# Performance work log

Measured on AMD Instinct MI355X. Metric: run time of the kernel, lower is better.

The kernel has to match this reference:

```python
import jax, jax.numpy as jnp
import numpy as np

B, T, D, H = 8, 4096, 1024, 16
DK = D // H
CHUNK = 64
E, TOPK, MULT, CAPF = 8, 2, 4, 1.25
HID = D * MULT
N = B * T
CAPACITY = int(CAPF * (N / E))  # 5120


def setup_inputs() -> dict:
    key = jax.random.key(0)
    ks = jax.random.split(key, 16)
    s = 0.02
    r = lambda k, shape: jax.random.normal(k, shape, jnp.float32) * s
    return {
        "x": jax.random.normal(ks[0], (B, T, D), jnp.float32),
        "norm1_scale": jnp.ones((D,), jnp.float32),
        "norm2_scale": jnp.ones((D,), jnp.float32),
        "Wq": r(ks[1], (D, D)), "bq": jnp.zeros((D,), jnp.float32),
        "Wk": r(ks[2], (D, D)), "bk": jnp.zeros((D,), jnp.float32),
        "Wv": r(ks[3], (D, D)), "bv": jnp.zeros((D,), jnp.float32),
        "Wg": r(ks[4], (D, D)), "bg": jnp.zeros((D,), jnp.float32),
        "Wo": r(ks[5], (D, D)), "bo": jnp.zeros((D,), jnp.float32),
        "router_W": r(ks[6], (D, E)), "router_b": jnp.zeros((E,), jnp.float32),
        "W1": r(ks[7], (E, D, HID)), "b1": jnp.zeros((E, HID), jnp.float32),
        "W2": r(ks[8], (E, HID, D)), "b2": jnp.zeros((E, D), jnp.float32),
    }


def rmsnorm(x, scale):
    # torch: x / (||x|| / sqrt(d)) * scale == x * rsqrt(mean(x^2)) * scale (no eps)
    return x / jnp.sqrt(jnp.mean(x * x, axis=-1, keepdims=True)) * scale


def apply_rope(x):
    # x: (B, H, T, DK); non-interleaved half-rotation as in source
    half = x.shape[-1] // 2
    t = x.shape[2]
    inv = 1.0 / (10000.0 ** (jnp.arange(half, dtype=jnp.float32) / half))
    ang = jnp.arange(t, dtype=jnp.float32)[:, None] * inv[None, :]  # (T, half)
    sin, cos = jnp.sin(ang)[None, None], jnp.cos(ang)[None, None]
    x1, x2 = x[..., :half], x[..., half:]
    return jnp.concatenate([x1 * cos - x2 * sin, x1 * sin + x2 * cos], axis=-1)


def phi(x):
    return jax.nn.elu(x) + 1.0


def attention(x, Wq, bq, Wk, bk, Wv, bv, Wg, bg, Wo, bo):
    b, t, c = x.shape
    heads = lambda y: y.reshape(b, t, H, DK).transpose(0, 2, 1, 3)  # (B,H,T,DK)
    q = phi(apply_rope(heads(x @ Wq + bq)))
    k = phi(apply_rope(heads(x @ Wk + bk)))
    v = heads(x @ Wv + bv)
    g = heads(jax.nn.sigmoid(x @ Wg + bg))
    nc = t // CHUNK
    to_chunks = lambda y: y.reshape(b, H, nc, CHUNK, DK).transpose(2, 0, 1, 3, 4)
    qs, ks_, vs, gs = map(to_chunks, (q, k, v, g))  # (nc,B,H,chunk,DK)
    S0 = jnp.zeros((b, H, DK, DK), x.dtype)
    Z0 = jnp.zeros((b, H, DK), x.dtype)

    def step(carry, inp):
        S, Z = carry
        qc, kc, vc, gc = inp
        S = S + jnp.einsum('bhtd,bhte->bhde', kc, vc)
        Z = Z + kc.sum(axis=2)
        num = jnp.einsum('bhtd,bhde->bhte', qc, S)
        den = jnp.einsum('bhtd,bhd->bht', qc, Z)[..., None] + 1e-6
        return (S, Z), gc * (num / den)

    _, outs = jax.lax.scan(step, (S0, Z0), (qs, ks_, vs, gs))  # (nc,B,H,chunk,DK)
    out = outs.transpose(1, 2, 0, 3, 4).reshape(b, H, t, DK)
    out = out.transpose(0, 2, 1, 3).reshape(b, t, c)
    return out @ Wo + bo


def moe(x, router_W, router_b, W1, b1, W2, b2):
    b, t, c = x.shape
    n = b * t
    xf = x.reshape(n, c)
    probs = jax.nn.softmax(xf @ router_W + router_b, axis=-1)
    topk_probs, topk_idx = jax.lax.top_k(probs, TOPK)
    topk_probs = topk_probs / topk_probs.sum(axis=-1, keepdims=True)
    out = jnp.zeros_like(xf)
    load = []
    for eid in range(E):  # fixed small expert loop (matches source structure)
        mask = (topk_idx == eid).reshape(-1)  # row-major == torch.where order
        idx = jnp.nonzero(mask, size=CAPACITY, fill_value=n * TOPK)[0]
        valid = idx < n * TOPK
        idxc = jnp.minimum(idx, n * TOPK - 1)
        tok, choice = idxc // TOPK, idxc % TOPK
        h = jax.nn.gelu(xf[tok] @ W1[eid] + b1[eid], approximate=False) @ W2[eid] + b2[eid]
        gate = jnp.where(valid, topk_probs[tok, choice], 0.0)
        out = out.at[tok].add(gate[:, None] * h)  # invalid slots have gate==0
        load.append(jnp.minimum(mask.sum(), CAPACITY).astype(xf.dtype))
    load = jnp.stack(load)
    importance = probs.sum(axis=0)
    importance = importance / importance.sum()
    load = load / load.sum()
    aux = (importance * load).sum() * (E ** 2)
    return out.reshape(b, t, c), aux


def reference(x, norm1_scale, norm2_scale, Wq, bq, Wk, bk, Wv, bv, Wg, bg, Wo, bo,
              router_W, router_b, W1, b1, W2, b2):
    x = x + attention(rmsnorm(x, norm1_scale), Wq, bq, Wk, bk, Wv, bv, Wg, bg, Wo, bo)
    moe_out, aux = moe(rmsnorm(x, norm2_scale), router_W, router_b, W1, b1, W2, b2)
    return (x + moe_out, aux)
```

## Files before the change

kernel.cpp:

```cpp
#include <hip/hip_runtime.h>
#include <hip/hip_bf16.h>

#define NTOK 32768
#define TSEQ 4096
#define DM   1024
#define NHEAD 16
#define NEXP 8
#define CAPE 5120
#define HIDN 4096
#define GTOK 8192
#define KSPL 5120

#ifndef __has_builtin
#define __has_builtin(x) 0
#endif
#if __has_builtin(__builtin_amdgcn_global_load_lds)
#define HAVE_GLOAD 1
#else
#define HAVE_GLOAD 0
#endif

typedef __attribute__((ext_vector_type(8))) short bf16x8;
typedef __attribute__((ext_vector_type(4))) float f32x4;

__device__ __forceinline__ float phi_f(float v) { return v > 0.f ? v + 1.f : expf(v); }

__device__ __forceinline__ unsigned short f2bf_bits(float f) {
    __hip_bfloat16 h = __float2bfloat16(f);
    union { __hip_bfloat16 h; unsigned short s; } u;
    u.h = h;
    return u.s;
}
__device__ __forceinline__ float bf_to_f(unsigned short s) {
    unsigned int u = ((unsigned int)s) << 16;
    union { unsigned int u; float f; } w; w.u = u;
    return w.f;
}

__global__ void k_ws_flag(float* out, float v) { if (threadIdx.x == 0) out[0] = v; }

__global__ void k_zero(int* p, int n) {
    int i = blockIdx.x * 256 + threadIdx.x;
    if (i < n) p[i] = 0;
}

__global__ __launch_bounds__(256) void k_rope_table(float* __restrict__ ct, float* __restrict__ st)
{
    const int idx = blockIdx.x * 256 + threadIdx.x;
    const int t = idx >> 5, j = idx & 31;
    const float inv = (float)(1.0 / pow(10000.0, (double)j / 32.0));
    float sn, cn;
    sincosf((float)t * inv, &sn, &cn);
    ct[idx] = cn; st[idx] = sn;
}

struct WPack { const float* W[5]; };
__global__ __launch_bounds__(256) void k_build_wstack(WPack P, __hip_bfloat16* __restrict__ BTbase)
{
    __shared__ float t_[32][33];
    const int z = blockIdx.z;
    const float* Wm = P.W[z];
    __hip_bfloat16* BT = BTbase + (size_t)z * DM * KSPL;
    const int n0 = blockIdx.x * 32, k0 = blockIdx.y * 32;
    const int c = threadIdx.x & 31, r0 = (threadIdx.x >> 5);
#pragma unroll
    for (int i = 0; i < 4; ++i) { int r = r0 + i * 8; t_[r][c] = Wm[(size_t)(k0 + r) * DM + n0 + c]; }
    __syncthreads();
#pragma unroll
    for (int i = 0; i < 4; ++i) {
        int r = r0 + i * 8;
        float val = t_[c][r];
        unsigned short b0 = f2bf_bits(val);
        float res = val - bf_to_f(b0);
        unsigned short b1 = f2bf_bits(res);
        __hip_bfloat16 h0, h1;
        union { __hip_bfloat16 h; unsigned short s; } u0, u1;
        u0.s = b0; u1.s = b1; h0 = u0.h; h1 = u1.h;
        const size_t nrow = (size_t)(n0 + r) * KSPL + (k0 + c);
        BT[nrow]            = h0;
        BT[nrow + 1024]     = h0;
        BT[nrow + 2048]     = h0;
        BT[nrow + 3072]     = h1;
        BT[nrow + 4096]     = h1;
    }
}

template<bool NORM>
__global__ __launch_bounds__(256) void k_rms_split(const float* __restrict__ X,
                                                   const float* __restrict__ nscale,
                                                   __hip_bfloat16* __restrict__ Xs)
{
    const int row = blockIdx.x;
    const int tid = threadIdx.x;
    const float* xr = X + (size_t)row * DM;
    float4 v = ((const float4*)xr)[tid];
    float r = 1.f;
    if (NORM) {
        float s = v.x * v.x + v.y * v.y + v.z * v.z + v.w * v.w;
        for (int off = 32; off; off >>= 1) s += __shfl_xor(s, off);
        __shared__ float redw[4];
        __shared__ float rbc;
        if ((tid & 63) == 0) redw[tid >> 6] = s;
        __syncthreads();
        if (tid == 0) {
            float tot = redw[0] + redw[1] + redw[2] + redw[3];
            rbc = (float)(1.0 / sqrt((double)tot * (1.0 / 1024.0)));
        }
        __syncthreads();
        r = rbc;
    }
    float c[4] = {v.x, v.y, v.z, v.w};
    if (NORM) {
        float4 ns = ((const float4*)nscale)[tid];
        c[0] *= r * ns.x; c[1] *= r * ns.y; c[2] *= r * ns.z; c[3] *= r * ns.w;
    }
    ushort4 p0, p1, p2;
    unsigned short* q0 = (unsigned short*)&p0;
    unsigned short* q1 = (unsigned short*)&p1;
    unsigned short* q2 = (unsigned short*)&p2;
#pragma unroll
    for (int i = 0; i < 4; ++i) {
        float x = c[i];
        unsigned short b0 = f2bf_bits(x);
        float r1 = x - bf_to_f(b0);
        unsigned short b1 = f2bf_bits(r1);
        float r2 = r1 - bf_to_f(b1);
        unsigned short b2 = f2bf_bits(r2);
        q0[i] = b0; q1[i] = b1; q2[i] = b2;
    }
    __hip_bfloat16* base = Xs + (size_t)row * 3072;
    ((ushort4*)(base))[tid] = p0;
    ((ushort4*)(base + 1024))[tid] = p1;
    ((ushort4*)(base + 2048))[tid] = p2;
}

__global__ __launch_bounds__(256) void k_rmsnorm_stats(const float* __restrict__ X,
                                                       float* __restrict__ rn,
                                                       const float* __restrict__ nscale,
                                                       __hip_bfloat16* __restrict__ xbf)
{
    const int row = blockIdx.x;
    const int tid = threadIdx.x;
    const float* xr = X + (size_t)row * DM;
    float4 v = ((const float4*)xr)[tid];
    float s = v.x * v.x + v.y * v.y + v.z * v.z + v.w * v.w;
    for (int off = 32; off; off >>= 1) s += __shfl_xor(s, off);
    __shared__ float redw[4];
    __shared__ float rbc;
    if ((tid & 63) == 0) redw[tid >> 6] = s;
    __syncthreads();
    if (tid == 0) {
        float tot = redw[0] + redw[1] + redw[2] + redw[3];
        float r = (float)(1.0 / sqrt((double)tot * (1.0 / 1024.0)));
        rn[row] = r; rbc = r;
    }
    __syncthreads();
    float r = rbc;
    float4 ns = ((const float4*)nscale)[tid];
    ushort4 o;
    o.x = f2bf_bits(v.x * r * ns.x);
    o.y = f2bf_bits(v.y * r * ns.y);
    o.z = f2bf_bits(v.z * r * ns.z);
    o.w = f2bf_bits(v.w * r * ns.w);
    ((ushort4*)(xbf + (size_t)row * DM))[tid] = o;
}

#if HAVE_GLOAD
__device__ __forceinline__ void gload16(const __hip_bfloat16* g, __hip_bfloat16* l)
{
    __builtin_amdgcn_global_load_lds((const __attribute__((address_space(1))) unsigned int*)g,
                                     (__attribute__((address_space(3))) unsigned int*)l, 16, 0, 0);
}
#endif

struct ProjPack {
    const __hip_bfloat16* BT[4];
    const float* bias[4];
    float* C[4];
};

template<int NMAT, bool RESID>
__global__ __launch_bounds__(256) void k_gemm_proj(const __hip_bfloat16* __restrict__ A,
                                                   ProjPack P,
                                                   const float* __restrict__ resid)
{
    const int z = (NMAT == 4) ? blockIdx.z : 0;
    const __hip_bfloat16* BT = P.BT[z];
    const float* bias = P.bias[z];
    float* C = P.C[z];
    const int m0 = blockIdx.y * 128;
    const int n0 = blockIdx.x * 128;
    const int tid = threadIdx.x;
    __shared__ alignas(16) __hip_bfloat16 As[128 * 32];
    __shared__ alignas(16) __hip_bfloat16 Bs[128 * 32];

    const int lane = tid & 63, wv = tid >> 6;
    const int lr = lane & 15, lgp = lane >> 4;
    const int wm = (wv >> 1) * 64, wn = (wv & 1) * 64;

#if HAVE_GLOAD
    const int rA0 = wv * 32 + (lane >> 2), rA1 = rA0 + 16;
    const int ch = lane & 3;
    const __hip_bfloat16* srcA0 = A + (size_t)(m0 + rA0) * 3072 + ((ch ^ (rA0 & 3)) * 8);
    const __hip_bfloat16* srcA1 = A + (size_t)(m0 + rA1) * 3072 + ((ch ^ (rA1 & 3)) * 8);
    const __hip_bfloat16* srcB0 = BT + (size_t)(n0 + rA0) * KSPL + ((ch ^ (rA0 & 3)) * 8);
    const __hip_bfloat16* srcB1 = BT + (size_t)(n0 + rA1) * KSPL + ((ch ^ (rA1 & 3)) * 8);
    __hip_bfloat16* ldsA0 = As + (size_t)(wv * 32) * 32;
    __hip_bfloat16* ldsA1 = As + (size_t)(wv * 32 + 16) * 32;
    __hip_bfloat16* ldsB0 = Bs + (size_t)(wv * 32) * 32;
    __hip_bfloat16* ldsB1 = Bs + (size_t)(wv * 32 + 16) * 32;
#else
    const int ar = tid >> 1, ac0 = (tid & 1) * 2;
    const __hip_bfloat16* Arow = A + (size_t)(m0 + ar) * 3072;
    const __hip_bfloat16* Brow = BT + (size_t)(n0 + ar) * KSPL;
#endif

    f32x4 acc[4][4];
#pragma unroll
    for (int i = 0; i < 4; ++i)
#pragma unroll
        for (int j = 0; j < 4; ++j) acc[i][j] = (f32x4){0.f, 0.f, 0.f, 0.f};

    int a_off[4], b_off[4];
#pragma unroll
    for (int i = 0; i < 4; ++i) {
        int mrow = wm + i * 16 + lr;
        a_off[i] = mrow * 32 + ((lgp ^ (mrow & 3)) * 8);
        int nrow = wn + i * 16 + lr;
        b_off[i] = nrow * 32 + ((lgp ^ (nrow & 3)) * 8);
    }

    for (int k0 = 0; k0 < KSPL; k0 += 32) {
        const int acol = (k0 < 3072) ? k0 : (k0 - 3072);
        __syncthreads();
#if HAVE_GLOAD
        gload16(srcA0 + acol, ldsA0);
        gload16(srcA1 + acol, ldsA1);
        gload16(srcB0 + k0, ldsB0);
        gload16(srcB1 + k0, ldsB1);
#else
        {
            uint4 av0 = *(const uint4*)(Arow + acol + ac0 * 8);
            uint4 av1 = *(const uint4*)(Arow + acol + ac0 * 8 + 8);
            uint4 bv0 = *(const uint4*)(Brow + k0 + ac0 * 8);
            uint4 bv1 = *(const uint4*)(Brow + k0 + ac0 * 8 + 8);
            *(uint4*)(As + ar * 32 + ((ac0    ) ^ (ar & 3)) * 8) = av0;
            *(uint4*)(As + ar * 32 + ((ac0 + 1) ^ (ar & 3)) * 8) = av1;
            *(uint4*)(Bs + ar * 32 + ((ac0    ) ^ (ar & 3)) * 8) = bv0;
            *(uint4*)(Bs + ar * 32 + ((ac0 + 1) ^ (ar & 3)) * 8) = bv1;
        }
#endif
        __syncthreads();
        bf16x8 af[4], bfr[4];
#pragma unroll
        for (int i = 0; i < 4; ++i) af[i] = *(const bf16x8*)(As + a_off[i]);
#pragma unroll
        for (int j = 0; j < 4; ++j) bfr[j] = *(const bf16x8*)(Bs + b_off[j]);
#pragma unroll
        for (int i = 0; i < 4; ++i)
#pragma unroll
            for (int j = 0; j < 4; ++j)
                acc[i][j] = __builtin_amdgcn_mfma_f32_16x16x32_bf16(af[i], bfr[j], acc[i][j], 0, 0, 0);
    }

#pragma unroll
    for (int i = 0; i < 4; ++i)
#pragma unroll
        for (int j = 0; j < 4; ++j) {
            const int col = n0 + wn + j * 16 + lr;
            const float bval = bias[col];
#pragma unroll
            for (int r = 0; r < 4; ++r) {
                const int rloc = wm + i * 16 + lgp * 4 + r;
                float v = acc[i][j][r] + bval;
                if (RESID) v += resid[(size_t)(m0 + rloc) * DM + col];
                C[(size_t)(m0 + rloc) * DM + col] = v;
            }
        }
}

__global__ __launch_bounds__(256) void k_scan_kv(float* KS, float* Vz,
                                                 const float* __restrict__ ct,
                                                 const float* __restrict__ st)
{
    const int c = blockIdx.x, bh = blockIdx.y;
    const int h = bh & 15, b = bh >> 4;
    const int tid = threadIdx.x;
    __shared__ float ks[64][68];
    __shared__ float vs[64][68];
    const size_t rowbase = ((size_t)b * TSEQ + c * 64) * DM + h * 64;
#pragma unroll
    for (int p = 0; p < 8; ++p) {
        int idx = p * 256 + tid;
        int t = idx >> 5, j = idx & 31;
        const size_t base = rowbase + (size_t)t * DM + j;
        float cn = ct[(c * 64 + t) * 32 + j];
        float sn = st[(c * 64 + t) * 32 + j];
        float k1 = KS[base], k2 = KS[base + 32];
        ks[t][j]      = phi_f(k1 * cn - k2 * sn);
        ks[t][j + 32] = phi_f(k1 * sn + k2 * cn);
    }
#pragma unroll
    for (int p = 0; p < 4; ++p) {
        int idx = p * 256 + tid;
        int t = idx >> 4, e4 = (idx & 15) * 4;
        *(float4*)&vs[t][e4] = *(const float4*)&Vz[rowbase + (size_t)t * DM + e4];
    }
    __syncthreads();
    const int e = tid & 63, dg = tid >> 6;
    float acc[16] = {};
    for (int t = 0; t < 64; ++t) {
        float vv = vs[t][e];
#pragma unroll
        for (int q = 0; q < 4; ++q) {
            float4 kq = *(const float4*)&ks[t][dg * 16 + q * 4];
            acc[q * 4 + 0] = fmaf(kq.x, vv, acc[q * 4 + 0]);
            acc[q * 4 + 1] = fmaf(kq.y, vv, acc[q * 4 + 1]);
            acc[q * 4 + 2] = fmaf(kq.z, vv, acc[q * 4 + 2]);
            acc[q * 4 + 3] = fmaf(kq.w, vv, acc[q * 4 + 3]);
        }
    }
#pragma unroll
    for (int i = 0; i < 16; ++i) {
        int d = dg * 16 + i;
        KS[rowbase + (size_t)d * DM + e] = acc[i];
    }
    if (tid < 64) {
        float z = 0.f;
        for (int t = 0; t < 64; ++t) z += ks[t][tid];
        Vz[rowbase + tid] = z;
    }
}

__global__ __launch_bounds__(256) void k_scan_prefix(float* S)
{
    const int sg = blockIdx.x, bh = blockIdx.y;
    const int h = bh & 15, b = bh >> 4;
    const int idx = sg * 256 + threadIdx.x;
    const int d = idx >> 6, e = idx & 63;
    const size_t base = (size_t)b * TSEQ * DM + h * 64 + (size_t)d * DM + e;
    float acc = 0.f;
    for (int c = 0; c < 64; ++c) {
        size_t p = base + (size_t)c * 64 * DM;
        acc += S[p];
        S[p] = acc;
    }
}

__global__ void k_zprefix(float* Vz)
{
    const int bh = blockIdx.x;
    const int h = bh & 15, b = bh >> 4;
    const int d = threadIdx.x;
    const size_t base = (size_t)b * TSEQ * DM + h * 64 + d;
    float acc = 0.f;
    for (int c = 0; c < 64; ++c) {
        size_t p = base + (size_t)c * 64 * DM;
        acc += Vz[p];
        Vz[p] = acc;
    }
}

__global__ __launch_bounds__(256) void k_scan_out(const float* __restrict__ Q,
                                                  const float* __restrict__ S,
                                                  const float* __restrict__ Zv,
                                                  float* GO,
                                                  const float* __restrict__ ct,
                                                  const float* __restrict__ st)
{
    const int c = blockIdx.x, bh = blockIdx.y;
    const int h = bh & 15, b = bh >> 4;
    const int tid = threadIdx.x;
    __shared__ float qs[64][69];
    __shared__ float Ss[64][68];
    __shared__ float den[64], Zl[64];
    const size_t rowbase = ((size_t)b * TSEQ + c * 64) * DM + h * 64;
#pragma unroll
    for (int p = 0; p < 8; ++p) {
        int idx = p * 256 + tid;
        int t = idx >> 5, j = idx & 31;
        const size_t base = rowbase + (size_t)t * DM + j;
        float cn = ct[(c * 64 + t) * 32 + j];
        float sn = st[(c * 64 + t) * 32 + j];
        float q1 = Q[base], q2 = Q[base + 32];
        qs[t][j]      = phi_f(q1 * cn - q2 * sn);
        qs[t][j + 32] = phi_f(q1 * sn + q2 * cn);
    }
#pragma unroll
    for (int p = 0; p < 4; ++p) {
        int idx = p * 256 + tid;
        int d = idx >> 4, e4 = (idx & 15) * 4;
        *(float4*)&Ss[d][e4] = *(const float4*)&S[rowbase + (size_t)d * DM + e4];
    }
    const int e = tid & 63, tg = tid >> 6;
    float greg[16];
#pragma unroll
    for (int i = 0; i < 16; ++i)
        greg[i] = GO[rowbase + (size_t)(tg * 16 + i) * DM + e];
    if (tid < 64) Zl[tid] = Zv[rowbase + tid];
    __syncthreads();
    if (tid < 64) {
        float dd = 0.f;
        for (int d = 0; d < 64; ++d) dd += qs[tid][d] * Zl[d];
        den[tid] = dd + 1e-6f;
    }
    __syncthreads();
    float acc[16] = {};
    for (int d = 0; d < 64; ++d) {
        float sv = Ss[d][e];
#pragma unroll
        for (int i = 0; i < 16; ++i)
            acc[i] = fmaf(qs[tg * 16 + i][d], sv, acc[i]);
    }
#pragma unroll
    for (int i = 0; i < 16; ++i) {
        int t = tg * 16 + i;
        float g = 1.f / (1.f + expf(-greg[i]));
        GO[rowbase + (size_t)t * DM + e] = g * acc[i] / den[t];
    }
}

__global__ __launch_bounds__(256) void k_router(const float* __restrict__ X2,
                                                const float* __restrict__ rn2,
                                                const float* __restrict__ ns2,
                                                const float* __restrict__ rW,
                                                const float* __restrict__ rb,
                                                int* __restrict__ route_e,
                                                float* __restrict__ route_g,
                                                float* __restrict__ probs)
{
    const int tok = blockIdx.x * 4 + (threadIdx.x >> 6);
    const int lane = threadIdx.x & 63;
    const float* xr = X2 + (size_t)tok * DM;
    const float rn = rn2[tok];
    float lg[8] = {};
    for (int d = lane; d < DM; d += 64) {
        float xv = xr[d] * rn * ns2[d];
        const float4* w4 = (const float4*)(rW + (size_t)d * 8);
        float4 w0 = w4[0], w1 = w4[1];
        lg[0] += xv * w0.x; lg[1] += xv * w0.y; lg[2] += xv * w0.z; lg[3] += xv * w0.w;
        lg[4] += xv * w1.x; lg[5] += xv * w1.y; lg[6] += xv * w1.z; lg[7] += xv * w1.w;
    }
#pragma unroll
    for (int e = 0; e < 8; ++e)
        for (int off = 32; off; off >>= 1) lg[e] += __shfl_xor(lg[e], off);
    if (lane == 0) {
        float pe[8]; float mx = -1e30f, s = 0.f;
#pragma unroll
        for (int e = 0; e < 8; ++e) { lg[e] += rb[e]; mx = fmaxf(mx, lg[e]); }
#pragma unroll
        for (int e = 0; e < 8; ++e) { pe[e] = expf(lg[e] - mx); s += pe[e]; }
#pragma unroll
        for (int e = 0; e < 8; ++e) { pe[e] /= s; probs[(size_t)tok * 8 + e] = pe[e]; }
        int i1 = 0; float p1 = pe[0];
#pragma unroll
        for (int e = 1; e < 8; ++e) if (pe[e] > p1) { p1 = pe[e]; i1 = e; }
        int i2 = -1; float p2 = -1.f;
#pragma unroll
        for (int e = 0; e < 8; ++e) if (e != i1 && pe[e] > p2) { p2 = pe[e]; i2 = e; }
        const float gsum = p1 + p2;
        route_e[tok * 2] = i1; route_e[tok * 2 + 1] = i2;
        route_g[tok * 2] = p1 / gsum; route_g[tok * 2 + 1] = p2 / gsum;
    }
}

__global__ __launch_bounds__(256) void k_count(const int* __restrict__ route_e, int* __restrict__ bcnt)
{
    __shared__ int c[8];
    const int tid = threadIdx.x;
    if (tid < 8) c[tid] = 0;
    __syncthreads();
    atomicAdd(&c[route_e[blockIdx.x * 256 + tid]], 1);
    __syncthreads();
    if (tid < 8) bcnt[blockIdx.x * 8 + tid] = c[tid];
}

__global__ void k_scan_blocks(const int* __restrict__ bcnt, int* __restrict__ bbase, int* __restrict__ ctot)
{
    const int e = threadIdx.x;
    if (e < 8) {
        int run = 0;
        for (int b = 0; b < 256; ++b) { bbase[b * 8 + e] = run; run += bcnt[b * 8 + e]; }
        ctot[e] = run;
    }
}

__global__ __launch_bounds__(256) void k_place(const int* __restrict__ route_e,
                                               const float* __restrict__ route_g,
                                               const int* __restrict__ bbase,
                                               int* __restrict__ tokslot,
                                               float* __restrict__ gateslot)
{
    const int tid = threadIdx.x;
    const int a = blockIdx.x * 256 + tid;
    const int e = route_e[a];
    __shared__ int se[256];
    se[tid] = e;
    __syncthreads();
    int rank = 0;
    for (int j = 0; j < tid; ++j) rank += (se[j] == e) ? 1 : 0;
    const int slot = bbase[blockIdx.x * 8 + e] + rank;
    if (slot < CAPE) {
        tokslot[e * CAPE + slot] = a >> 1;
        gateslot[e * CAPE + slot] = route_g[a];
    }
}

__global__ __launch_bounds__(256) void k_aux(const float* __restrict__ probs,
                                             const int* __restrict__ ctot,
                                             float* __restrict__ out_aux)
{
    const int tid = threadIdx.x;
    float part[8] = {};
    for (int i = tid; i < NTOK; i += 256) {
        const float* p = probs + (size_t)i * 8;
#pragma unroll
        for (int e = 0; e < 8; ++e) part[e] += p[e];
    }
    __shared__ float red[256];
    __shared__ float accs[8];
    for (int e = 0; e < 8; ++e) {
        red[tid] = part[e];
        __syncthreads();
        for (int s = 128; s; s >>= 1) { if (tid < s) red[tid] += red[tid + s]; __syncthreads(); }
        if (tid == 0) accs[e] = red[0];
        __syncthreads();
    }
    if (tid == 0) {
        float isum = 0.f, lsum = 0.f, l[8];
        for (int e = 0; e < 8; ++e) isum += accs[e];
        for (int e = 0; e < 8; ++e) { l[e] = fminf((float)ctot[e], (float)CAPE); lsum += l[e]; }
        float aux = 0.f;
        for (int e = 0; e < 8; ++e) aux += (accs[e] / isum) * (l[e] / lsum);
        out_aux[0] = aux * 64.f;
    }
}

__global__ void k_transpose_bf16(const float* __restrict__ src, __hip_bfloat16* __restrict__ dst,
                                 int K_, int N_)
{
    __shared__ float t_[32][33];
    const int z = blockIdx.z;
    const float* s = src + (size_t)z * K_ * N_;
    __hip_bfloat16* d = dst + (size_t)z * K_ * N_;
    const int n0 = blockIdx.x * 32, k0 = blockIdx.y * 32;
    const int c = threadIdx.x, r0 = threadIdx.y;
#pragma unroll
    for (int i = 0; i < 4; ++i) { int r = r0 + i * 8; t_[r][c] = s[(size_t)(k0 + r) * N_ + n0 + c]; }
    __syncthreads();
#pragma unroll
    for (int i = 0; i < 4; ++i) { int r = r0 + i * 8; d[(size_t)(n0 + r) * K_ + k0 + c] = __float2bfloat16(t_[c][r]); }
}

template<int MODE>
__global__ __launch_bounds__(256) void k_gemm_bf16(const __hip_bfloat16* __restrict__ A,
                                                   const __hip_bfloat16* __restrict__ BT,
                                                   const float* __restrict__ bias,
                                                   __hip_bfloat16* __restrict__ Hout,
                                                   float* __restrict__ Fout,
                                                   const int* __restrict__ tokslot,
                                                   const float* __restrict__ gateslot,
                                                   int K, int Nout, int e0)
{
    const int le = blockIdx.z;
    const int e = e0 + le;
    const int m0 = blockIdx.y * 128;
    const int n0 = blockIdx.x * 128;
    const int tid = threadIdx.x;
    __shared__ alignas(16) __hip_bfloat16 As[128 * 32];
    __shared__ alignas(16) __hip_bfloat16 Bs[128 * 32];
    __shared__ int s_tok[128];
    __shared__ float s_gate[128];
    if (tid < 128) {
        s_tok[tid] = tokslot[e * CAPE + m0 + tid];
        s_gate[tid] = gateslot[e * CAPE + m0 + tid];
    }
    __syncthreads();

    const int lane = tid & 63, wv = tid >> 6;
    const int lr = lane & 15, lgp = lane >> 4;
    const int wm = (wv >> 1) * 64, wn = (wv & 1) * 64;

#if HAVE_GLOAD
    const int rA0 = wv * 32 + (lane >> 2), rA1 = rA0 + 16;
    const int ch = lane & 3;
    const __hip_bfloat16 *srcA0, *srcA1;
    if (MODE == 0) {
        srcA0 = A + (size_t)s_tok[rA0] * K + ((ch ^ (rA0 & 3)) * 8);
        srcA1 = A + (size_t)s_tok[rA1] * K + ((ch ^ (rA1 & 3)) * 8);
    } else {
        srcA0 = A + ((size_t)le * CAPE + m0 + rA0) * K + ((ch ^ (rA0 & 3)) * 8);
        srcA1 = A + ((size_t)le * CAPE + m0 + rA1) * K + ((ch ^ (rA1 & 3)) * 8);
    }
    const __hip_bfloat16* srcB0 = BT + ((size_t)e * Nout + n0 + rA0) * K + ((ch ^ (rA0 & 3)) * 8);
    const __hip_bfloat16* srcB1 = BT + ((size_t)e * Nout + n0 + rA1) * K + ((ch ^ (rA1 & 3)) * 8);
    __hip_bfloat16* ldsA0 = As + (size_t)(wv * 32) * 32;
    __hip_bfloat16* ldsA1 = As + (size_t)(wv * 32 + 16) * 32;
    __hip_bfloat16* ldsB0 = Bs + (size_t)(wv * 32) * 32;
    __hip_bfloat16* ldsB1 = Bs + (size_t)(wv * 32 + 16) * 32;
#else
    const int ar = tid >> 1, ac0 = (tid & 1) * 2;
    const __hip_bfloat16* Arow;
    if (MODE == 0) Arow = A + (size_t)s_tok[ar] * K;
    else           Arow = A + ((size_t)le * CAPE + m0 + ar) * K;
    const __hip_bfloat16* Brow = BT + ((size_t)e * Nout + n0 + ar) * K;
#endif

    f32x4 acc[4][4];
#pragma unroll
    for (int i = 0; i < 4; ++i)
#pragma unroll
        for (int j = 0; j < 4; ++j) acc[i][j] = (f32x4){0.f, 0.f, 0.f, 0.f};

    int a_off[4], b_off[4];
#pragma unroll
    for (int i = 0; i < 4; ++i) {
        int mrow = wm + i * 16 + lr;
        a_off[i] = mrow * 32 + ((lgp ^ (mrow & 3)) * 8);
        int nrow = wn + i * 16 + lr;
        b_off[i] = nrow * 32 + ((lgp ^ (nrow & 3)) * 8);
    }

    for (int k0 = 0; k0 < K; k0 += 32) {
        __syncthreads();
#if HAVE_GLOAD
        gload16(srcA0 + k0, ldsA0);
        gload16(srcA1 + k0, ldsA1);
        gload16(srcB0 + k0, ldsB0);
        gload16(srcB1 + k0, ldsB1);
#else
        {
            uint4 av0 = *(const uint4*)(Arow + k0 + ac0 * 8);
            uint4 av1 = *(const uint4*)(Arow + k0 + ac0 * 8 + 8);
            uint4 bv0 = *(const uint4*)(Brow + k0 + ac0 * 8);
            uint4 bv1 = *(const uint4*)(Brow + k0 + ac0 * 8 + 8);
            *(uint4*)(As + ar * 32 + ((ac0    ) ^ (ar & 3)) * 8) = av0;
            *(uint4*)(As + ar * 32 + ((ac0 + 1) ^ (ar & 3)) * 8) = av1;
            *(uint4*)(Bs + ar * 32 + ((ac0    ) ^ (ar & 3)) * 8) = bv0;
            *(uint4*)(Bs + ar * 32 + ((ac0 + 1) ^ (ar & 3)) * 8) = bv1;
        }
#endif
        __syncthreads();
        bf16x8 af[4], bfr[4];
#pragma unroll
        for (int i = 0; i < 4; ++i) af[i] = *(const bf16x8*)(As + a_off[i]);
#pragma unroll
        for (int j = 0; j < 4; ++j) bfr[j] = *(const bf16x8*)(Bs + b_off[j]);
#pragma unroll
        for (int i = 0; i < 4; ++i)
#pragma unroll
            for (int j = 0; j < 4; ++j)
                acc[i][j] = __builtin_amdgcn_mfma_f32_16x16x32_bf16(af[i], bfr[j], acc[i][j], 0, 0, 0);
    }

#pragma unroll
    for (int i = 0; i < 4; ++i)
#pragma unroll
        for (int j = 0; j < 4; ++j) {
            const int col = n0 + wn + j * 16 + lr;
            const float bval = bias[(size_t)e * Nout + col];
#pragma unroll
            for (int r = 0; r < 4; ++r) {
                const int rloc = wm + i * 16 + lgp * 4 + r;
                float v = acc[i][j][r] + bval;
                if (MODE == 0) {
                    v = 0.5f * v * (1.f + erff(v * 0.70710678118654752f));
                    Hout[((size_t)le * CAPE + m0 + rloc) * Nout + col] = __float2bfloat16(v);
                } else {
                    const float g = s_gate[rloc];
                    if (g != 0.f) atomicAdd(&Fout[(size_t)s_tok[rloc] * DM + col], v * g);
                }
            }
        }
}

extern "C" void kernel_launch(void* const* d_in, const int* in_sizes, int n_in,
                              void* d_out, int out_size, void* d_ws, size_t ws_size,
                              hipStream_t stream)
{
    (void)in_sizes; (void)n_in; (void)out_size;
    const float* x   = (const float*)d_in[0];
    const float* ns1 = (const float*)d_in[1];
    const float* ns2 = (const float*)d_in[2];
    const float* Wq  = (const float*)d_in[3];
    const float* bq  = (const float*)d_in[4];
    const float* Wk  = (const float*)d_in[5];
    const float* bk  = (const float*)d_in[6];
    const float* Wv  = (const float*)d_in[7];
    const float* bv  = (const float*)d_in[8];
    const float* Wg  = (const float*)d_in[9];
    const float* bg  = (const float*)d_in[10];
    const float* Wo  = (const float*)d_in[11];
    const float* bo  = (const float*)d_in[12];
    const float* rW  = (const float*)d_in[13];
    const float* rb  = (const float*)d_in[14];
    const float* W1  = (const float*)d_in[15];
    const float* b1  = (const float*)d_in[16];
    const float* W2  = (const float*)d_in[17];
    const float* b2  = (const float*)d_in[18];
    float* out = (float*)d_out;
    char* wsb = (char*)d_ws;

    constexpr size_t MiB = 1024ull * 1024ull;
    constexpr size_t R = (size_t)NTOK * DM * 4;
    constexpr size_t TAIL = 3 * R;
    constexpr size_t OFF_RN1  = TAIL;
    constexpr size_t OFF_RN2  = OFF_RN1 + (size_t)NTOK * 4;
    constexpr size_t OFF_PROB = OFF_RN2 + (size_t)NTOK * 4;
    constexpr size_t OFF_RE   = OFF_PROB + (size_t)NTOK * 8 * 4;
    constexpr size_t OFF_RG   = OFF_RE + (size_t)NTOK * 2 * 4;
    constexpr size_t OFF_BCNT = OFF_RG + (size_t)NTOK * 2 * 4;
    constexpr size_t OFF_BBASE= OFF_BCNT + 256 * 8 * 4;
    constexpr size_t OFF_CTOT = OFF_BBASE + 256 * 8 * 4;
    constexpr size_t OFF_TOK  = OFF_CTOT + 4096;
    constexpr size_t OFF_GATE = OFF_TOK + (size_t)NEXP * CAPE * 4;
    constexpr size_t REQUIRED = OFF_GATE + (size_t)NEXP * CAPE * 4;

    if (ws_size < REQUIRED) {
        k_ws_flag<<<1, 64, 0, stream>>>(out, (float)(ws_size >> 20));
        return;
    }

    __hip_bfloat16* xn2bf = (__hip_bfloat16*)(wsb);
    __hip_bfloat16* WST   = (__hip_bfloat16*)(wsb + 64 * MiB);
    __hip_bfloat16* Xs    = (__hip_bfloat16*)(wsb + 114 * MiB);
    float* qg = (float*)(wsb + 162 * MiB);
    float* kg = (float*)(wsb + 194 * MiB);
    float* gg = (float*)(wsb + 226 * MiB);
    __hip_bfloat16* W1T  = (__hip_bfloat16*)(wsb + 64 * MiB);
    __hip_bfloat16* W2T  = (__hip_bfloat16*)(wsb + 128 * MiB);
    __hip_bfloat16* Hbuf = (__hip_bfloat16*)(wsb + 192 * MiB);

    float* rn2 = (float*)(wsb + OFF_RN2);
    float* probs = (float*)(wsb + OFF_PROB);
    float* rope_ct = (float*)(wsb + OFF_PROB);
    float* rope_st = (float*)(wsb + OFF_PROB + (size_t)TSEQ * 32 * 4);
    int*   route_e = (int*)(wsb + OFF_RE);
    float* route_g = (float*)(wsb + OFF_RG);
    int*   bcnt  = (int*)(wsb + OFF_BCNT);
    int*   bbase = (int*)(wsb + OFF_BBASE);
    int*   ctot  = (int*)(wsb + OFF_CTOT);
    int*   tokslot  = (int*)(wsb + OFF_TOK);
    float* gateslot = (float*)(wsb + OFF_GATE);

    k_rope_table<<<512, 256, 0, stream>>>(rope_ct, rope_st);
    {
        WPack WP; WP.W[0] = Wq; WP.W[1] = Wk; WP.W[2] = Wg; WP.W[3] = Wv; WP.W[4] = Wo;
        k_build_wstack<<<dim3(32, 32, 5), 256, 0, stream>>>(WP, WST);
    }

    for (int gi = 0; gi < 4; ++gi) {
        const size_t tok0 = (size_t)gi * GTOK;
        const float* xg = x + tok0 * DM;
        float* vg = out + tok0 * DM;

        k_rms_split<true><<<GTOK, 256, 0, stream>>>(xg, ns1, Xs);

        ProjPack P;
        P.BT[0] = WST;                     P.bias[0] = bq; P.C[0] = qg;
        P.BT[1] = WST + (size_t)DM * KSPL; P.bias[1] = bk; P.C[1] = kg;
        P.BT[2] = WST + 2ull * DM * KSPL;  P.bias[2] = bg; P.C[2] = gg;
        P.BT[3] = WST + 3ull * DM * KSPL;  P.bias[3] = bv; P.C[3] = vg;
        k_gemm_proj<4, false><<<dim3(8, GTOK / 128, 4), 256, 0, stream>>>(Xs, P, nullptr);

        k_scan_kv<<<dim3(64, 32), 256, 0, stream>>>(kg, vg, rope_ct, rope_st);
        k_scan_prefix<<<dim3(16, 32), 256, 0, stream>>>(kg);
        k_zprefix<<<32, 64, 0, stream>>>(vg);
        k_scan_out<<<dim3(64, 32), 256, 0, stream>>>(qg, kg, vg, gg, rope_ct, rope_st);

        k_rms_split<false><<<GTOK, 256, 0, stream>>>(gg, nullptr, Xs);

        ProjPack P2;
        P2.BT[0] = WST + 4ull * DM * KSPL; P2.bias[0] = bo; P2.C[0] = vg;
        P2.BT[1] = P2.BT[2] = P2.BT[3] = P2.BT[0];
        P2.bias[1] = P2.bias[2] = P2.bias[3] = bo;
        P2.C[1] = P2.C[2] = P2.C[3] = vg;
        k_gemm_proj<1, true><<<dim3(8, GTOK / 128, 1), 256, 0, stream>>>(Xs, P2, xg);

        k_rmsnorm_stats<<<GTOK, 256, 0, stream>>>(vg, rn2 + tok0, ns2, xn2bf + tok0 * DM);
    }

    k_router<<<NTOK / 4, 256, 0, stream>>>(out, rn2, ns2, rW, rb, route_e, route_g, probs);

    k_count<<<256, 256, 0, stream>>>(route_e, bcnt);
    k_scan_blocks<<<1, 64, 0, stream>>>(bcnt, bbase, ctot);
    k_zero<<<(NEXP * CAPE * 2 + 255) / 256, 256, 0, stream>>>(tokslot, NEXP * CAPE * 2);
    k_place<<<256, 256, 0, stream>>>(route_e, route_g, bbase, tokslot, gateslot);

    k_aux<<<1, 256, 0, stream>>>(probs, ctot, out + (size_t)NTOK * DM);

    k_transpose_bf16<<<dim3(HIDN / 32, DM / 32, NEXP), dim3(32, 8), 0, stream>>>(W1, W1T, DM, HIDN);
    k_transpose_bf16<<<dim3(DM / 32, HIDN / 32, NEXP), dim3(32, 8), 0, stream>>>(W2, W2T, HIDN, DM);

    for (int g = 0; g < 3; ++g) {
        const int e0 = g * 3;
        const int ecnt = (g == 2) ? 2 : 3;
        k_gemm_bf16<0><<<dim3(HIDN / 128, CAPE / 128, ecnt), 256, 0, stream>>>(
            xn2bf, W1T, b1, Hbuf, nullptr, tokslot, gateslot, DM, HIDN, e0);
        k_gemm_bf16<1><<<dim3(DM / 128, CAPE / 128, ecnt), 256, 0, stream>>>(
            Hbuf, W2T, b2, nullptr, out, tokslot, gateslot, HIDN, DM, e0);
    }
}
```

Before: 4.618 ms.

## Use fragment-major LDS layout with K=64 steps and fuse split into scan_out

Both GEMM kernels now stage A and B tiles in shared memory in MFMA-fragment-major order ([2][8][512]) and advance K by 64 per barrier pair, halving the number of syncs. Each lane now reads its bf16x8 fragment contiguously instead of through XOR-swizzled offsets. Separately, k_scan_out now writes the gated output directly as a three-way bf16 split into the Xs buffer. This removes a separate k_rms_split pass and a float round trip through global memory. The cost is doubled LDS per block, which may reduce occupancy.

```diff
diff --git a/kernel.cpp b/kernel.cpp
--- a/kernel.cpp
+++ b/kernel.cpp
@@ -173,6 +173,7 @@
 }
 #endif
 
+
 struct ProjPack {
     const __hip_bfloat16* BT[4];
     const float* bias[4];
@@ -191,29 +192,28 @@
     const int m0 = blockIdx.y * 128;
     const int n0 = blockIdx.x * 128;
     const int tid = threadIdx.x;
-    __shared__ alignas(16) __hip_bfloat16 As[128 * 32];
-    __shared__ alignas(16) __hip_bfloat16 Bs[128 * 32];
+    __shared__ alignas(16) __hip_bfloat16 As[2][8][512];
+    __shared__ alignas(16) __hip_bfloat16 Bs[2][8][512];
 
     const int lane = tid & 63, wv = tid >> 6;
+    const int p = wv >> 1, q = wv & 1;
     const int lr = lane & 15, lgp = lane >> 4;
-    const int wm = (wv >> 1) * 64, wn = (wv & 1) * 64;
-
-#if HAVE_GLOAD
-    const int rA0 = wv * 32 + (lane >> 2), rA1 = rA0 + 16;
-    const int ch = lane & 3;
-    const __hip_bfloat16* srcA0 = A + (size_t)(m0 + rA0) * 3072 + ((ch ^ (rA0 & 3)) * 8);
-    const __hip_bfloat16* srcA1 = A + (size_t)(m0 + rA1) * 3072 + ((ch ^ (rA1 & 3)) * 8);
-    const __hip_bfloat16* srcB0 = BT + (size_t)(n0 + rA0) * KSPL + ((ch ^ (rA0 & 3)) * 8);
-    const __hip_bfloat16* srcB1 = BT + (size_t)(n0 + rA1) * KSPL + ((ch ^ (rA1 & 3)) * 8);
-    __hip_bfloat16* ldsA0 = As + (size_t)(wv * 32) * 32;
-    __hip_bfloat16* ldsA1 = As + (size_t)(wv * 32 + 16) * 32;
-    __hip_bfloat16* ldsB0 = Bs + (size_t)(wv * 32) * 32;
-    __hip_bfloat16* ldsB1 = Bs + (size_t)(wv * 32 + 16) * 32;
-#else
-    const int ar = tid >> 1, ac0 = (tid & 1) * 2;
-    const __hip_bfloat16* Arow = A + (size_t)(m0 + ar) * 3072;
-    const __hip_bfloat16* Brow = BT + (size_t)(n0 + ar) * KSPL;
-#endif
+
+    const __hip_bfloat16* srcA[4];
+    const __hip_bfloat16* srcB[4];
+    __hip_bfloat16* dstA[4];
+    __hip_bfloat16* dstB[4];
+#pragma unroll
+    for (int f4 = 0; f4 < 4; ++f4) {
+        const int fA = q * 4 + f4;
+        const int arow = m0 + p * 64 + (fA >> 1) * 16 + lr;
+        srcA[f4] = A + (size_t)arow * 3072 + (fA & 1) * 32 + lgp * 8;
+        dstA[f4] = &As[p][fA][0];
+        const int fB = p * 4 + f4;
+        const int brow = n0 + q * 64 + (fB >> 1) * 16 + lr;
+        srcB[f4] = BT + (size_t)brow * KSPL + (fB & 1) * 32 + lgp * 8;
+        dstB[f4] = &Bs[q][fB][0];
+    }
 
     f32x4 acc[4][4];
 #pragma unroll
@@ -221,48 +221,39 @@
 #pragma unroll
         for (int j = 0; j < 4; ++j) acc[i][j] = (f32x4){0.f, 0.f, 0.f, 0.f};
 
-    int a_off[4], b_off[4];
-#pragma unroll
-    for (int i = 0; i < 4; ++i) {
-        int mrow = wm + i * 16 + lr;
-        a_off[i] = mrow * 32 + ((lgp ^ (mrow & 3)) * 8);
-        int nrow = wn + i * 16 + lr;
-        b_off[i] = nrow * 32 + ((lgp ^ (nrow & 3)) * 8);
-    }
-
-    for (int k0 = 0; k0 < KSPL; k0 += 32) {
+    for (int k0 = 0; k0 < KSPL; k0 += 64) {
         const int acol = (k0 < 3072) ? k0 : (k0 - 3072);
         __syncthreads();
 #if HAVE_GLOAD
-        gload16(srcA0 + acol, ldsA0);
-        gload16(srcA1 + acol, ldsA1);
-        gload16(srcB0 + k0, ldsB0);
-        gload16(srcB1 + k0, ldsB1);
+#pragma unroll
+        for (int f4 = 0; f4 < 4; ++f4) {
+            gload16(srcA[f4] + acol, dstA[f4]);
+            gload16(srcB[f4] + k0, dstB[f4]);
+        }
 #else
-        {
-            uint4 av0 = *(const uint4*)(Arow + acol + ac0 * 8);
-            uint4 av1 = *(const uint4*)(Arow + acol + ac0 * 8 + 8);
-            uint4 bv0 = *(const uint4*)(Brow + k0 + ac0 * 8);
-            uint4 bv1 = *(const uint4*)(Brow + k0 + ac0 * 8 + 8);
-            *(uint4*)(As + ar * 32 + ((ac0    ) ^ (ar & 3)) * 8) = av0;
-            *(uint4*)(As + ar * 32 + ((ac0 + 1) ^ (ar & 3)) * 8) = av1;
-            *(uint4*)(Bs + ar * 32 + ((ac0    ) ^ (ar & 3)) * 8) = bv0;
-            *(uint4*)(Bs + ar * 32 + ((ac0 + 1) ^ (ar & 3)) * 8) = bv1;
+#pragma unroll
+        for (int f4 = 0; f4 < 4; ++f4) {
+            *(uint4*)(dstA[f4] + (size_t)lane * 8) = *(const uint4*)(srcA[f4] + acol);
+            *(uint4*)(dstB[f4] + (size_t)lane * 8) = *(const uint4*)(srcB[f4] + k0);
         }
 #endif
         __syncthreads();
-        bf16x8 af[4], bfr[4];
-#pragma unroll
-        for (int i = 0; i < 4; ++i) af[i] = *(const bf16x8*)(As + a_off[i]);
-#pragma unroll
-        for (int j = 0; j < 4; ++j) bfr[j] = *(const bf16x8*)(Bs + b_off[j]);
-#pragma unroll
-        for (int i = 0; i < 4; ++i)
-#pragma unroll
-            for (int j = 0; j < 4; ++j)
-                acc[i][j] = __builtin_amdgcn_mfma_f32_16x16x32_bf16(af[i], bfr[j], acc[i][j], 0, 0, 0);
-    }
-
+#pragma unroll
+        for (int kk = 0; kk < 2; ++kk) {
+            bf16x8 af[4], bfr[4];
+#pragma unroll
+            for (int i = 0; i < 4; ++i) af[i] = *(const bf16x8*)&As[p][i * 2 + kk][lane * 8];
+#pragma unroll
+            for (int j = 0; j < 4; ++j) bfr[j] = *(const bf16x8*)&Bs[q][j * 2 + kk][lane * 8];
+#pragma unroll
+            for (int i = 0; i < 4; ++i)
+#pragma unroll
+                for (int j = 0; j < 4; ++j)
+                    acc[i][j] = __builtin_amdgcn_mfma_f32_16x16x32_bf16(af[i], bfr[j], acc[i][j], 0, 0, 0);
+        }
+    }
+
+    const int wm = p * 64, wn = q * 64;
 #pragma unroll
     for (int i = 0; i < 4; ++i)
 #pragma unroll
@@ -275,6 +266,111 @@
                 float v = acc[i][j][r] + bval;
                 if (RESID) v += resid[(size_t)(m0 + rloc) * DM + col];
                 C[(size_t)(m0 + rloc) * DM + col] = v;
+            }
+        }
+}
+
+template<int MODE>
+__global__ __launch_bounds__(256) void k_gemm_bf16(const __hip_bfloat16* __restrict__ A,
+                                                   const __hip_bfloat16* __restrict__ BT,
+                                                   const float* __restrict__ bias,
+                                                   __hip_bfloat16* __restrict__ Hout,
+                                                   float* __restrict__ Fout,
+                                                   const int* __restrict__ tokslot,
+                                                   const float* __restrict__ gateslot,
+                                                   int K, int Nout, int e0)
+{
+    const int le = blockIdx.z;
+    const int e = e0 + le;
+    const int m0 = blockIdx.y * 128;
+    const int n0 = blockIdx.x * 128;
+    const int tid = threadIdx.x;
+    __shared__ alignas(16) __hip_bfloat16 As[2][8][512];
+    __shared__ alignas(16) __hip_bfloat16 Bs[2][8][512];
+    __shared__ int s_tok[128];
+    __shared__ float s_gate[128];
+    if (tid < 128) {
+        s_tok[tid] = tokslot[e * CAPE + m0 + tid];
+        s_gate[tid] = gateslot[e * CAPE + m0 + tid];
+    }
+    __syncthreads();
+
+    const int lane = tid & 63, wv = tid >> 6;
+    const int p = wv >> 1, q = wv & 1;
+    const int lr = lane & 15, lgp = lane >> 4;
+
+    const __hip_bfloat16* srcA[4];
+    const __hip_bfloat16* srcB[4];
+    __hip_bfloat16* dstA[4];
+    __hip_bfloat16* dstB[4];
+#pragma unroll
+    for (int f4 = 0; f4 < 4; ++f4) {
+        const int fA = q * 4 + f4;
+        const int arl = p * 64 + (fA >> 1) * 16 + lr;
+        if (MODE == 0) srcA[f4] = A + (size_t)s_tok[arl] * K + (fA & 1) * 32 + lgp * 8;
+        else           srcA[f4] = A + ((size_t)le * CAPE + m0 + arl) * K + (fA & 1) * 32 + lgp * 8;
+        dstA[f4] = &As[p][fA][0];
+        const int fB = p * 4 + f4;
+        const int brow = n0 + q * 64 + (fB >> 1) * 16 + lr;
+        srcB[f4] = BT + ((size_t)e * Nout + brow) * K + (fB & 1) * 32 + lgp * 8;
+        dstB[f4] = &Bs[q][fB][0];
+    }
+
+    f32x4 acc[4][4];
+#pragma unroll
+    for (int i = 0; i < 4; ++i)
+#pragma unroll
+        for (int j = 0; j < 4; ++j) acc[i][j] = (f32x4){0.f, 0.f, 0.f, 0.f};
+
+    for (int k0 = 0; k0 < K; k0 += 64) {
+        __syncthreads();
+#if HAVE_GLOAD
+#pragma unroll
+        for (int f4 = 0; f4 < 4; ++f4) {
+            gload16(srcA[f4] + k0, dstA[f4]);
+            gload16(srcB[f4] + k0, dstB[f4]);
+        }
+#else
+#pragma unroll
+        for (int f4 = 0; f4 < 4; ++f4) {
+            *(uint4*)(dstA[f4] + (size_t)lane * 8) = *(const uint4*)(srcA[f4] + k0);
+            *(uint4*)(dstB[f4] + (size_t)lane * 8) = *(const uint4*)(srcB[f4] + k0);
+        }
+#endif
+        __syncthreads();
+#pragma unroll
+        for (int kk = 0; kk < 2; ++kk) {
+            bf16x8 af[4], bfr[4];
+#pragma unroll
+            for (int i = 0; i < 4; ++i) af[i] = *(const bf16x8*)&As[p][i * 2 + kk][lane * 8];
+#pragma unroll
+            for (int j = 0; j < 4; ++j) bfr[j] = *(const bf16x8*)&Bs[q][j * 2 + kk][lane * 8];
+#pragma unroll
+            for (int i = 0; i < 4; ++i)
+#pragma unroll
+                for (int j = 0; j < 4; ++j)
+                    acc[i][j] = __builtin_amdgcn_mfma_f32_16x16x32_bf16(af[i], bfr[j], acc[i][j], 0, 0, 0);
+        }
+    }
+
+    const int wm = p * 64, wn = q * 64;
+#pragma unroll
+    for (int i = 0; i < 4; ++i)
+#pragma unroll
+        for (int j = 0; j < 4; ++j) {
+            const int col = n0 + wn + j * 16 + lr;
+            const float bval = bias[(size_t)e * Nout + col];
+#pragma unroll
+            for (int r = 0; r < 4; ++r) {
+                const int rloc = wm + i * 16 + lgp * 4 + r;
+                float v = acc[i][j][r] + bval;
+                if (MODE == 0) {
+                    v = 0.5f * v * (1.f + erff(v * 0.70710678118654752f));
+                    Hout[((size_t)le * CAPE + m0 + rloc) * Nout + col] = __float2bfloat16(v);
+                } else {
+                    const float g = s_gate[rloc];
+                    if (g != 0.f) atomicAdd(&Fout[(size_t)s_tok[rloc] * DM + col], v * g);
+                }
             }
         }
 }
@@ -312,12 +408,12 @@
     for (int t = 0; t < 64; ++t) {
         float vv = vs[t][e];
 #pragma unroll
-        for (int q = 0; q < 4; ++q) {
-            float4 kq = *(const float4*)&ks[t][dg * 16 + q * 4];
-            acc[q * 4 + 0] = fmaf(kq.x, vv, acc[q * 4 + 0]);
-            acc[q * 4 + 1] = fmaf(kq.y, vv, acc[q * 4 + 1]);
-            acc[q * 4 + 2] = fmaf(kq.z, vv, acc[q * 4 + 2]);
-            acc[q * 4 + 3] = fmaf(kq.w, vv, acc[q * 4 + 3]);
+        for (int qq = 0; qq < 4; ++qq) {
+            float4 kq = *(const float4*)&ks[t][dg * 16 + qq * 4];
+            acc[qq * 4 + 0] = fmaf(kq.x, vv, acc[qq * 4 + 0]);
+            acc[qq * 4 + 1] = fmaf(kq.y, vv, acc[qq * 4 + 1]);
+            acc[qq * 4 + 2] = fmaf(kq.z, vv, acc[qq * 4 + 2]);
+            acc[qq * 4 + 3] = fmaf(kq.w, vv, acc[qq * 4 + 3]);
         }
     }
 #pragma unroll
@@ -364,7 +460,8 @@
 __global__ __launch_bounds__(256) void k_scan_out(const float* __restrict__ Q,
                                                   const float* __restrict__ S,
                                                   const float* __restrict__ Zv,
-                                                  float* GO,
+                                                  const float* __restrict__ G,
+                                                  __hip_bfloat16* __restrict__ Xs,
                                                   const float* __restrict__ ct,
                                                   const float* __restrict__ st)
 {
@@ -396,7 +493,7 @@
     float greg[16];
 #pragma unroll
     for (int i = 0; i < 16; ++i)
-        greg[i] = GO[rowbase + (size_t)(tg * 16 + i) * DM + e];
+        greg[i] = G[rowbase + (size_t)(tg * 16 + i) * DM + e];
     if (tid < 64) Zl[tid] = Zv[rowbase + tid];
     __syncthreads();
     if (tid < 64) {
@@ -412,11 +509,21 @@
         for (int i = 0; i < 16; ++i)
             acc[i] = fmaf(qs[tg * 16 + i][d], sv, acc[i]);
     }
+    unsigned short* Xu = (unsigned short*)Xs;
 #pragma unroll
     for (int i = 0; i < 16; ++i) {
         int t = tg * 16 + i;
         float g = 1.f / (1.f + expf(-greg[i]));
-        GO[rowbase + (size_t)t * DM + e] = g * acc[i] / den[t];
+        float o = g * acc[i] / den[t];
+        unsigned short b0 = f2bf_bits(o);
+        float r1 = o - bf_to_f(b0);
+        unsigned short b1 = f2bf_bits(r1);
+        float r2 = r1 - bf_to_f(b1);
+        unsigned short b2 = f2bf_bits(r2);
+        const size_t xb = (size_t)(b * TSEQ + c * 64 + t) * 3072 + h * 64 + e;
+        Xu[xb] = b0;
+        Xu[xb + 1024] = b1;
+        Xu[xb + 2048] = b2;
     }
 }
 
@@ -550,128 +657,6 @@
     __syncthreads();
 #pragma unroll
     for (int i = 0; i < 4; ++i) { int r = r0 + i * 8; d[(size_t)(n0 + r) * K_ + k0 + c] = __float2bfloat16(t_[c][r]); }
-}
-
-template<int MODE>
-__global__ __launch_bounds__(256) void k_gemm_bf16(const __hip_bfloat16* __restrict__ A,
-                                                   const __hip_bfloat16* __restrict__ BT,
-                                                   const float* __restrict__ bias,
-                                                   __hip_bfloat16* __restrict__ Hout,
-                                                   float* __restrict__ Fout,
-                                                   const int* __restrict__ tokslot,
-                                                   const float* __restrict__ gateslot,
-                                                   int K, int Nout, int e0)
-{
-    const int le = blockIdx.z;
-    const int e = e0 + le;
-    const int m0 = blockIdx.y * 128;
-    const int n0 = blockIdx.x * 128;
-    const int tid = threadIdx.x;
-    __shared__ alignas(16) __hip_bfloat16 As[128 * 32];
-    __shared__ alignas(16) __hip_bfloat16 Bs[128 * 32];
-    __shared__ int s_tok[128];
-    __shared__ float s_gate[128];
-    if (tid < 128) {
-        s_tok[tid] = tokslot[e * CAPE + m0 + tid];
-        s_gate[tid] = gateslot[e * CAPE + m0 + tid];
-    }
-    __syncthreads();
-
-    const int lane = tid & 63, wv = tid >> 6;
-    const int lr = lane & 15, lgp = lane >> 4;
-    const int wm = (wv >> 1) * 64, wn = (wv & 1) * 64;
-
-#if HAVE_GLOAD
-    const int rA0 = wv * 32 + (lane >> 2), rA1 = rA0 + 16;
-    const int ch = lane & 3;
-    const __hip_bfloat16 *srcA0, *srcA1;
-    if (MODE == 0) {
-        srcA0 = A + (size_t)s_tok[rA0] * K + ((ch ^ (rA0 & 3)) * 8);
-        srcA1 = A + (size_t)s_tok[rA1] * K + ((ch ^ (rA1 & 3)) * 8);
-    } else {
-        srcA0 = A + ((size_t)le * CAPE + m0 + rA0) * K + ((ch ^ (rA0 & 3)) * 8);
-        srcA1 = A + ((size_t)le * CAPE + m0 + rA1) * K + ((ch ^ (rA1 & 3)) * 8);
-    }
-    const __hip_bfloat16* srcB0 = BT + ((size_t)e * Nout + n0 + rA0) * K + ((ch ^ (rA0 & 3)) * 8);
-    const __hip_bfloat16* srcB1 = BT + ((size_t)e * Nout + n0 + rA1) * K + ((ch ^ (rA1 & 3)) * 8);
-    __hip_bfloat16* ldsA0 = As + (size_t)(wv * 32) * 32;
-    __hip_bfloat16* ldsA1 = As + (size_t)(wv * 32 + 16) * 32;
-    __hip_bfloat16* ldsB0 = Bs + (size_t)(wv * 32) * 32;
-    __hip_bfloat16* ldsB1 = Bs + (size_t)(wv * 32 + 16) * 32;
-#else
-    const int ar = tid >> 1, ac0 = (tid & 1) * 2;
-    const __hip_bfloat16* Arow;
-    if (MODE == 0) Arow = A + (size_t)s_tok[ar] * K;
-    else           Arow = A + ((size_t)le * CAPE + m0 + ar) * K;
-    const __hip_bfloat16* Brow = BT + ((size_t)e * Nout + n0 + ar) * K;
-#endif
-
-    f32x4 acc[4][4];
-#pragma unroll
-    for (int i = 0; i < 4; ++i)
-#pragma unroll
-        for (int j = 0; j < 4; ++j) acc[i][j] = (f32x4){0.f, 0.f, 0.f, 0.f};
-
-    int a_off[4], b_off[4];
-#pragma unroll
-    for (int i = 0; i < 4; ++i) {
-        int mrow = wm + i * 16 + lr;
-        a_off[i] = mrow * 32 + ((lgp ^ (mrow & 3)) * 8);
-        int nrow = wn + i * 16 + lr;
-        b_off[i] = nrow * 32 + ((lgp ^ (nrow & 3)) * 8);
-    }
-
-    for (int k0 = 0; k0 < K; k0 += 32) {
-        __syncthreads();
-#if HAVE_GLOAD
-        gload16(srcA0 + k0, ldsA0);
-        gload16(srcA1 + k0, ldsA1);
-        gload16(srcB0 + k0, ldsB0);
-        gload16(srcB1 + k0, ldsB1);
-#else
-        {
-            uint4 av0 = *(const uint4*)(Arow + k0 + ac0 * 8);
-            uint4 av1 = *(const uint4*)(Arow + k0 + ac0 * 8 + 8);
-            uint4 bv0 = *(const uint4*)(Brow + k0 + ac0 * 8);
-            uint4 bv1 = *(const uint4*)(Brow + k0 + ac0 * 8 + 8);
-            *(uint4*)(As + ar * 32 + ((ac0    ) ^ (ar & 3)) * 8) = av0;
-            *(uint4*)(As + ar * 32 + ((ac0 + 1) ^ (ar & 3)) * 8) = av1;
-            *(uint4*)(Bs + ar * 32 + ((ac0    ) ^ (ar & 3)) * 8) = bv0;
-            *(uint4*)(Bs + ar * 32 + ((ac0 + 1) ^ (ar & 3)) * 8) = bv1;
-        }
-#endif
-        __syncthreads();
-        bf16x8 af[4], bfr[4];
-#pragma unroll
-        for (int i = 0; i < 4; ++i) af[i] = *(const bf16x8*)(As + a_off[i]);
-#pragma unroll
-        for (int j = 0; j < 4; ++j) bfr[j] = *(const bf16x8*)(Bs + b_off[j]);
-#pragma unroll
-        for (int i = 0; i < 4; ++i)
-#pragma unroll
-            for (int j = 0; j < 4; ++j)
-                acc[i][j] = __builtin_amdgcn_mfma_f32_16x16x32_bf16(af[i], bfr[j], acc[i][j], 0, 0, 0);
-    }
-
-#pragma unroll
-    for (int i = 0; i < 4; ++i)
-#pragma unroll
-        for (int j = 0; j < 4; ++j) {
-            const int col = n0 + wn + j * 16 + lr;
-            const float bval = bias[(size_t)e * Nout + col];
-#pragma unroll
-            for (int r = 0; r < 4; ++r) {
-                const int rloc = wm + i * 16 + lgp * 4 + r;
-                float v = acc[i][j][r] + bval;
-                if (MODE == 0) {
-                    v = 0.5f * v * (1.f + erff(v * 0.70710678118654752f));
-                    Hout[((size_t)le * CAPE + m0 + rloc) * Nout + col] = __float2bfloat16(v);
-                } else {
-                    const float g = s_gate[rloc];
-                    if (g != 0.f) atomicAdd(&Fout[(size_t)s_tok[rloc] * DM + col], v * g);
-                }
-            }
-        }
 }
 
 extern "C" void kernel_launch(void* const* d_in, const int* in_sizes, int n_in,
@@ -766,9 +751,7 @@
         k_scan_kv<<<dim3(64, 32), 256, 0, stream>>>(kg, vg, rope_ct, rope_st);
         k_scan_prefix<<<dim3(16, 32), 256, 0, stream>>>(kg);
         k_zprefix<<<32, 64, 0, stream>>>(vg);
-        k_scan_out<<<dim3(64, 32), 256, 0, stream>>>(qg, kg, vg, gg, rope_ct, rope_st);
-
-        k_rms_split<false><<<GTOK, 256, 0, stream>>>(gg, nullptr, Xs);
+        k_scan_out<<<dim3(64, 32), 256, 0, stream>>>(qg, kg, vg, gg, Xs, rope_ct, rope_st);
 
         ProjPack P2;
         P2.BT[0] = WST + 4ull * DM * KSPL; P2.bias[0] = bo; P2.C[0] = vg;
```

Measured after the change: 5.760 ms. +24.7%, slower.
